# Optimization experiments

Hardware: AMD Instinct MI355X
Metric: run time of the kernel (lower is better)

## Reference

```python
import jax, jax.numpy as jnp
import numpy as np

B, N, K, M, CIN, O, OUT = 4, 1024, 30, 8, 9, 64, 512
BN_SCALE = 1.0 / np.sqrt(1.0 + 1e-5)  # eval-mode BatchNorm with default stats/affine


def setup_inputs() -> dict:
    key = jax.random.key(0)
    ks = jax.random.split(key, 8)
    x = jax.random.normal(ks[0], (B, CIN, N), jnp.float32)
    norm_plt = jax.random.normal(ks[1], (B, 3, N), jnp.float32)
    cls_label = jnp.zeros((B, 16), jnp.float32)
    conv1_w = jax.random.normal(ks[2], (64, 18), jnp.float32) * np.sqrt(2.0 / 18.0)
    conv1_b = jnp.zeros((64,), jnp.float32)
    sn_hw = jax.random.normal(ks[3], (4, 16, 28), jnp.float32) * np.sqrt(2.0 / 28.0)
    sn_ow = jax.random.normal(ks[4], (4, M, 16), jnp.float32) * np.sqrt(2.0 / 16.0)
    sn_ob = jnp.zeros((4, M), jnp.float32)
    mats = jax.random.normal(ks[5], (4, 2 * O, M * O), jnp.float32) * np.sqrt(2.0 / (2.0 * O))
    convt_w = jax.random.normal(ks[6], (OUT, 5 * O), jnp.float32) * np.sqrt(2.0 / (5.0 * O))
    return dict(x=x, norm_plt=norm_plt, cls_label=cls_label, conv1_w=conv1_w,
                conv1_b=conv1_b, sn_hw=sn_hw, sn_ow=sn_ow, sn_ob=sn_ob,
                mats=mats, convt_w=convt_w)


def _gather(feat, idx):
    # feat (B,N,C), idx (B,N,K) int -> (B,N,K,C): neighbor feature gather
    return jax.vmap(lambda f, i: f[i])(feat, idx)


def _bn(t):
    return t * BN_SCALE


def reference(x, norm_plt, cls_label, conv1_w, conv1_b, sn_hw, sn_ow, sn_ob, mats, convt_w):
    xt = jnp.transpose(x, (0, 2, 1))                       # (B,N,9)
    sq = jnp.sum(xt * xt, axis=-1)
    neg_d = 2.0 * jnp.einsum('bic,bjc->bij', xt, xt) - sq[:, :, None] - sq[:, None, :]
    _, idx = jax.lax.top_k(neg_d, K)                       # (B,N,K) knn indices

    nbr = _gather(xt, idx)                                 # (B,N,K,9)
    ctr = jnp.broadcast_to(xt[:, :, None, :], nbr.shape)   # (B,N,K,9)
    diff = nbr - ctr
    ed = jnp.linalg.norm(diff, axis=-1, keepdims=True)     # (B,N,K,1)
    xyz = jnp.concatenate([diff, nbr, ctr, ed], axis=-1)   # (B,N,K,28) scorenet input

    # get_graph_feature -> conv1 (1x1) -> BN -> relu -> max over k
    gf = jnp.concatenate([diff, ctr], axis=-1)             # (B,N,K,18)
    h = jax.nn.relu(_bn(jnp.einsum('bnkc,oc->bnko', gf, conv1_w) + conv1_b))
    x1 = jnp.max(h, axis=2)                                # (B,N,64)

    feats = [x1]
    f = x1
    for l in range(4):  # PAConv layers 2..5 (sequential, fixed count)
        hid = jax.nn.relu(_bn(jnp.einsum('bnkc,hc->bnkh', xyz, sn_hw[l])))
        score = jax.nn.softmax(jnp.einsum('bnkh,mh->bnkm', hid, sn_ow[l]) + sn_ob[l], axis=-1)
        kern = mats[l]                                     # (128, M*64)
        # feat_trans_dgcnn: neighbor uses full kernel on [f;f], center uses top half
        point = (jnp.concatenate([f, f], axis=-1) @ kern).reshape(B, N, M, O)
        center = (f @ kern[:O]).reshape(B, N, M, O)
        # assemble_dgcnn: sum_k sum_m score * (point[knn] - center)
        gp = _gather(point.reshape(B, N, M * O), idx).reshape(B, N, K, M, O)
        out = jnp.einsum('bnkm,bnkmo->bno', score, gp) - jnp.einsum('bnkm,bnmo->bno', score, center)
        f = jax.nn.relu(_bn(out))
        feats.append(f)

    xx = jnp.concatenate(feats, axis=-1)                   # (B,N,320)
    xc = jax.nn.relu(_bn(jnp.einsum('bnc,oc->bno', xx, convt_w)))
    return jnp.max(xc, axis=1)                             # (B,512) global max pool
```

## Files before the change

### kernel.cpp

```cpp
#include <hip/hip_runtime.h>
#include <hip/hip_bf16.h>

#define B 4
#define N 1024
#define KNN 30
#define MM 8
#define OO 64
#define OUTC 512
#define HID 16
#define FD 320
#define BNS 0.9999950000374997f

typedef float f32x4 __attribute__((ext_vector_type(4)));
typedef short s16x8 __attribute__((ext_vector_type(8)));

#define OFF_XT     0
#define OFF_SQ     36864
#define OFF_IDX    40960
#define OFF_CVT    163840
#define OFF_K2T    245760
#define OFF_FB     376832
#define OFF_H      1032192

__global__ void __launch_bounds__(256) k_prep(const float* __restrict__ x,
                                              const float* __restrict__ convt_w,
                                              float* __restrict__ xt,
                                              float* __restrict__ sq,
                                              __hip_bfloat16* __restrict__ cvt_bf,
                                              float* __restrict__ out) {
  int id = blockIdx.x * 256 + threadIdx.x;
  if (id < B * N) {
    int b = id >> 10, n = id & 1023;
    float s = 0.f;
#pragma unroll
    for (int c = 0; c < 9; c++) {
      float v = x[(b * 9 + c) * N + n];
      xt[id * 9 + c] = v;
      s = fmaf(v, v, s);
    }
    sq[id] = s;
  }
  if (id < B * OUTC) out[id] = 0.f;
  if (id < 512 * 320) cvt_bf[id] = __float2bfloat16(convt_w[id]);
}

__global__ void __launch_bounds__(256) k_tpose(const float* __restrict__ mats,
                                               __hip_bfloat16* __restrict__ k2t_bf) {
  int blk = blockIdx.x;
  int l = blk >> 4, part = (blk >> 3) & 1, m = blk & 7;
  __shared__ float tile[64][65];
  int tr = threadIdx.x >> 6;
  int tc = threadIdx.x & 63;
  const float* src = mats + l * 65536 + (part * 64) * 512 + m * 64;
#pragma unroll
  for (int it = 0; it < 16; it++) {
    int c = it * 4 + tr;
    tile[c][tc] = src[c * 512 + tc];
  }
  __syncthreads();
  __hip_bfloat16* dst = k2t_bf + l * 65536 + part * 512 + m * 64;
#pragma unroll
  for (int it = 0; it < 16; it++) {
    int o = it * 4 + tr;
    dst[o * 1024 + tc] = __float2bfloat16(tile[tc][o]);
  }
}

__global__ void __launch_bounds__(256) k_knn(const float* __restrict__ xt,
                                             const float* __restrict__ sq,
                                             int* __restrict__ idx) {
  int r = threadIdx.x >> 6;
  int lane = threadIdx.x & 63;
  int row = blockIdx.x * 4 + r;
  int b = row >> 10;
  __shared__ unsigned int hist[4][256];
  __shared__ unsigned int cntr[4];
  __shared__ unsigned int bp[4];
  __shared__ int bn[4];
  const float* xb = xt + (b << 10) * 9;
  const float* sb = sq + (b << 10);
  float cx[9];
#pragma unroll
  for (int c = 0; c < 9; c++) cx[c] = xt[row * 9 + c];
  float sqn = sq[row];
  unsigned int key[16];
#pragma unroll
  for (int s = 0; s < 16; s++) {
    int j = s * 64 + lane;
    const float* xj = xb + j * 9;
    float dot = 0.f;
#pragma unroll
    for (int c = 0; c < 9; c++) dot = fmaf(cx[c], xj[c], dot);
    float v = 2.0f * dot - sqn - sb[j];
    unsigned int u = __float_as_uint(v);
    key[s] = u ^ ((unsigned int)(((int)u) >> 31) | 0x80000000u);
  }
  if (lane == 0) cntr[r] = 0;
  unsigned int prefix = 0;
  int need = KNN;
  for (int p = 0; p < 4; p++) {
    int shift = 24 - 8 * p;
    for (int i = lane; i < 256; i += 64) hist[r][i] = 0;
    __syncthreads();
    unsigned int himask = (p == 0) ? 0u : (0xFFFFFFFFu << (shift + 8));
#pragma unroll
    for (int s = 0; s < 16; s++) {
      if ((key[s] & himask) == prefix)
        atomicAdd(&hist[r][(key[s] >> shift) & 255], 1u);
    }
    __syncthreads();
    int c0 = hist[r][4 * lane + 0], c1 = hist[r][4 * lane + 1];
    int c2 = hist[r][4 * lane + 2], c3 = hist[r][4 * lane + 3];
    int lsum = c0 + c1 + c2 + c3;
    int sfx = lsum;
#pragma unroll
    for (int ofs = 1; ofs < 64; ofs <<= 1) {
      int t = __shfl_down(sfx, ofs, 64);
      if (lane + ofs < 64) sfx += t;
    }
    int A3 = sfx - lsum;
    int A2 = A3 + c3, A1 = A2 + c2, A0 = A1 + c1;
    if (A0 < need && need <= A0 + c0) { bp[r] = prefix | ((unsigned)(4 * lane + 0) << shift); bn[r] = need - A0; }
    if (A1 < need && need <= A1 + c1) { bp[r] = prefix | ((unsigned)(4 * lane + 1) << shift); bn[r] = need - A1; }
    if (A2 < need && need <= A2 + c2) { bp[r] = prefix | ((unsigned)(4 * lane + 2) << shift); bn[r] = need - A2; }
    if (A3 < need && need <= A3 + c3) { bp[r] = prefix | ((unsigned)(4 * lane + 3) << shift); bn[r] = need - A3; }
    __syncthreads();
    prefix = bp[r];
    need = bn[r];
  }
  unsigned int T = prefix;
  int above_total = KNN - need;
  int* orow = idx + row * KNN;
#pragma unroll
  for (int s = 0; s < 16; s++) {
    if (key[s] > T) {
      unsigned int pslot = atomicAdd(&cntr[r], 1u);
      orow[pslot] = s * 64 + lane;
    }
  }
  int base = 0;
  for (int s = 0; s < 16; s++) {
    unsigned long long m = __ballot(key[s] == T);
    if (key[s] == T) {
      int rk = base + __popcll(m & ((1ull << lane) - 1ull));
      if (rk < need) orow[above_total + rk] = s * 64 + lane;
    }
    base += __popcll(m);
    if (base >= need) break;
  }
}

__global__ void __launch_bounds__(64) k_conv1(const float* __restrict__ xt,
                                              const int* __restrict__ idx,
                                              const float* __restrict__ w,
                                              const float* __restrict__ bias,
                                              __hip_bfloat16* __restrict__ feats_bf) {
  int row = blockIdx.x;
  int t = threadIdx.x;
  int b = row >> 10;
  __shared__ float ws[64 * 18];
  __shared__ __align__(16) float diff_s[KNN][12];
  __shared__ float ctr_s[9];
  for (int i = t; i < 64 * 18; i += 64) ws[i] = w[i];
  if (t < 9) ctr_s[t] = xt[row * 9 + t];
  __syncthreads();
  if (t < KNN) {
    int j = idx[row * KNN + t];
    const float* xj = xt + ((b << 10) + j) * 9;
#pragma unroll
    for (int c = 0; c < 9; c++) diff_s[t][c] = xj[c] - ctr_s[c];
  }
  __syncthreads();
  float wd[9];
#pragma unroll
  for (int c = 0; c < 9; c++) wd[c] = ws[t * 18 + c];
  float cd = 0.f;
#pragma unroll
  for (int c = 0; c < 9; c++) cd = fmaf(ctr_s[c], ws[t * 18 + 9 + c], cd);
  float best = -3.0e38f;
  for (int k = 0; k < KNN; k++) {
    const float4* dr = (const float4*)diff_s[k];
    float4 d0 = dr[0], d1 = dr[1], d2v = dr[2];
    float dd = 0.f;
    dd = fmaf(d0.x, wd[0], dd); dd = fmaf(d0.y, wd[1], dd);
    dd = fmaf(d0.z, wd[2], dd); dd = fmaf(d0.w, wd[3], dd);
    dd = fmaf(d1.x, wd[4], dd); dd = fmaf(d1.y, wd[5], dd);
    dd = fmaf(d1.z, wd[6], dd); dd = fmaf(d1.w, wd[7], dd);
    dd = fmaf(d2v.x, wd[8], dd);
    best = fmaxf(best, dd);
  }
  float val = (best + cd + bias[t]) * BNS;
  feats_bf[row * FD + t] = __float2bfloat16(fmaxf(val, 0.f));
}

__global__ void __launch_bounds__(256) k_g(const float* __restrict__ xt,
                                           const int* __restrict__ idx,
                                           const float* __restrict__ hw,
                                           const float* __restrict__ ow,
                                           const float* __restrict__ ob,
                                           const __hip_bfloat16* __restrict__ feats_bf,
                                           __hip_bfloat16* __restrict__ H, int l) {
  int row0 = blockIdx.x * 4;
  int t = threadIdx.x;
  int b = row0 >> 10;
  __shared__ float hws[HID * 28];
  __shared__ float ows[MM * HID];
  __shared__ float obs[MM];
  __shared__ __align__(16) float sc[4][KNN][8];
  __shared__ __align__(16) float ssum[4][8];
  __shared__ int js[4][KNN];
  __shared__ float ctr[4][9];
  for (int i = t; i < HID * 28; i += 256) hws[i] = hw[l * HID * 28 + i];
  if (t < MM * HID) ows[t] = ow[l * MM * HID + t];
  if (t < MM) obs[t] = ob[l * MM + t];
  if (t < 36) { int r = t / 9, c = t - r * 9; ctr[r][c] = xt[(row0 + r) * 9 + c]; }
  if (t < 4 * KNN) {
    int r = t / KNN, k = t - r * KNN;
    js[r][k] = (b << 10) + idx[(row0 + r) * KNN + k];
  }
  __syncthreads();
  if (t < 4 * KNN) {
    int r = t / KNN, k = t - r * KNN;
    const float* xj = xt + js[r][k] * 9;
    float xv[28];
    float d2 = 0.f;
#pragma unroll
    for (int c = 0; c < 9; c++) {
      float nb = xj[c], ct = ctr[r][c], df = nb - ct;
      xv[c] = df; xv[9 + c] = nb; xv[18 + c] = ct;
      d2 = fmaf(df, df, d2);
    }
    xv[27] = sqrtf(d2);
    float hid[HID];
#pragma unroll
    for (int h = 0; h < HID; h++) {
      float a = 0.f;
#pragma unroll
      for (int c = 0; c < 28; c++) a = fmaf(xv[c], hws[h * 28 + c], a);
      hid[h] = fmaxf(a * BNS, 0.f);
    }
    float lg[MM], mx = -3.0e38f;
#pragma unroll
    for (int m = 0; m < MM; m++) {
      float a = obs[m];
#pragma unroll
      for (int h = 0; h < HID; h++) a = fmaf(hid[h], ows[m * HID + h], a);
      lg[m] = a; mx = fmaxf(mx, a);
    }
    float s = 0.f;
#pragma unroll
    for (int m = 0; m < MM; m++) { lg[m] = __expf(lg[m] - mx); s += lg[m]; }
    float inv = 1.0f / s;
#pragma unroll
    for (int m = 0; m < MM; m++) sc[r][k][m] = lg[m] * inv;
  }
  __syncthreads();
  if (t < 32) {
    int r = t >> 3, m = t & 7;
    float a = 0.f;
#pragma unroll
    for (int k = 0; k < KNN; k++) a += sc[r][k][m];
    ssum[r][m] = a;
  }
  __syncthreads();
  int r = t >> 6, c = t & 63;
  int row = row0 + r;
  float g[MM] = {};
  for (int k = 0; k < KNN; k++) {
    float fv = __bfloat162float(feats_bf[js[r][k] * FD + l * 64 + c]);
    const float4* s4 = (const float4*)sc[r][k];
    float4 s0 = s4[0], s1 = s4[1];
    g[0] = fmaf(s0.x, fv, g[0]); g[1] = fmaf(s0.y, fv, g[1]);
    g[2] = fmaf(s0.z, fv, g[2]); g[3] = fmaf(s0.w, fv, g[3]);
    g[4] = fmaf(s1.x, fv, g[4]); g[5] = fmaf(s1.y, fv, g[5]);
    g[6] = fmaf(s1.z, fv, g[6]); g[7] = fmaf(s1.w, fv, g[7]);
  }
  float fn = __bfloat162float(feats_bf[row * FD + l * 64 + c]);
  __hip_bfloat16* Hrow = H + row * 1024;
#pragma unroll
  for (int m = 0; m < MM; m++) {
    Hrow[m * 64 + c] = __float2bfloat16(g[m] - ssum[r][m] * fn);
    Hrow[512 + m * 64 + c] = __float2bfloat16(g[m]);
  }
}

__global__ void __launch_bounds__(64) k_hgemm(const __hip_bfloat16* __restrict__ H,
                                              const __hip_bfloat16* __restrict__ k2t_bf,
                                              __hip_bfloat16* __restrict__ feats_bf,
                                              int l) {
  int rb = blockIdx.x >> 2, cb = blockIdx.x & 3;
  int row0 = rb * 16, c0 = cb * 16;
  int lane = threadIdx.x;
  int lr = lane & 15, lk8 = (lane >> 4) * 8;
  const short* Hs = (const short*)H;
  const short* Ks = (const short*)(k2t_bf + l * 65536);
  const short* arow = Hs + (row0 + lr) * 1024 + lk8;
  const short* brow = Ks + (c0 + lr) * 1024 + lk8;
  f32x4 acc = {0.f, 0.f, 0.f, 0.f};
#pragma unroll 8
  for (int kk = 0; kk < 32; kk++) {
    s16x8 a = *(const s16x8*)(arow + kk * 32);
    s16x8 bb = *(const s16x8*)(brow + kk * 32);
    acc = __builtin_amdgcn_mfma_f32_16x16x32_bf16(a, bb, acc, 0, 0, 0);
  }
#pragma unroll
  for (int i = 0; i < 4; i++) {
    int row = row0 + (lane >> 4) * 4 + i;
    feats_bf[row * FD + (l + 1) * 64 + c0 + lr] =
        __float2bfloat16(fmaxf(acc[i] * BNS, 0.f));
  }
}

__global__ void __launch_bounds__(256) k_final(const __hip_bfloat16* __restrict__ feats_bf,
                                               const __hip_bfloat16* __restrict__ cvt_bf,
                                               float* __restrict__ out) {
  int m0 = (blockIdx.x >> 1) * 16;
  int nhalf = (blockIdx.x & 1) * 256;
  int w = threadIdx.x >> 6;
  int lane = threadIdx.x & 63;
  int lr = lane & 15, lk8 = (lane >> 4) * 8;
  int b = m0 >> 10;
  const short* Fs = (const short*)feats_bf;
  const short* Ws = (const short*)cvt_bf;
  const short* arow = Fs + (m0 + lr) * FD + lk8;
  int nbase = nhalf + w * 64;
  const short* brow = Ws + (nbase + lr) * FD + lk8;
  f32x4 acc[4] = {{0.f, 0.f, 0.f, 0.f}, {0.f, 0.f, 0.f, 0.f},
                  {0.f, 0.f, 0.f, 0.f}, {0.f, 0.f, 0.f, 0.f}};
#pragma unroll
  for (int kk = 0; kk < 10; kk++) {
    int k0 = kk * 32;
    s16x8 a = *(const s16x8*)(arow + k0);
#pragma unroll
    for (int tn = 0; tn < 4; tn++) {
      s16x8 bb = *(const s16x8*)(brow + tn * 16 * FD + k0);
      acc[tn] = __builtin_amdgcn_mfma_f32_16x16x32_bf16(a, bb, acc[tn], 0, 0, 0);
    }
  }
#pragma unroll
  for (int tn = 0; tn < 4; tn++) {
    float mx = fmaxf(fmaxf(acc[tn][0], acc[tn][1]), fmaxf(acc[tn][2], acc[tn][3]));
    mx = fmaxf(mx, __shfl_xor(mx, 16, 64));
    mx = fmaxf(mx, __shfl_xor(mx, 32, 64));
    if ((lane >> 4) == 0) {
      float val = fmaxf(mx * BNS, 0.f);
      int o = nbase + tn * 16 + lr;
      atomicMax((unsigned int*)out + b * OUTC + o, __float_as_uint(val));
    }
  }
}

extern "C" void kernel_launch(void* const* d_in, const int* in_sizes, int n_in,
                              void* d_out, int out_size, void* d_ws, size_t ws_size,
                              hipStream_t stream) {
  const float* x       = (const float*)d_in[0];
  const float* conv1_w = (const float*)d_in[3];
  const float* conv1_b = (const float*)d_in[4];
  const float* sn_hw   = (const float*)d_in[5];
  const float* sn_ow   = (const float*)d_in[6];
  const float* sn_ob   = (const float*)d_in[7];
  const float* mats    = (const float*)d_in[8];
  const float* convt_w = (const float*)d_in[9];
  float* out = (float*)d_out;

  float* w = (float*)d_ws;
  float* xt = w + OFF_XT;
  float* sq = w + OFF_SQ;
  int* idx = (int*)(w + OFF_IDX);
  __hip_bfloat16* cvt_bf = (__hip_bfloat16*)(w + OFF_CVT);
  __hip_bfloat16* k2t_bf = (__hip_bfloat16*)(w + OFF_K2T);
  __hip_bfloat16* feats_bf = (__hip_bfloat16*)(w + OFF_FB);
  __hip_bfloat16* H = (__hip_bfloat16*)(w + OFF_H);

  k_prep<<<640, 256, 0, stream>>>(x, convt_w, xt, sq, cvt_bf, out);
  k_tpose<<<64, 256, 0, stream>>>(mats, k2t_bf);
  k_knn<<<1024, 256, 0, stream>>>(xt, sq, idx);
  k_conv1<<<4096, 64, 0, stream>>>(xt, idx, conv1_w, conv1_b, feats_bf);
  for (int l = 0; l < 4; l++) {
    k_g<<<1024, 256, 0, stream>>>(xt, idx, sn_hw, sn_ow, sn_ob, feats_bf, H, l);
    k_hgemm<<<1024, 64, 0, stream>>>(H, k2t_bf, feats_bf, l);
  }
  k_final<<<512, 256, 0, stream>>>(feats_bf, cvt_bf, out);
}
```

Measured before the change: 216.0 us.

## Fuse score/gather and H-GEMM into one per-layer kernel with LDS-resident H

Merges k_g and k_hgemm into a single k_layer kernel. Each block handles 16 rows, builds the H tile in shared memory and runs the MFMA GEMM directly from LDS, so the global H round-trip and four launches go away. It also folds the mats transpose into k_prep and batches k_conv1 to 4 rows per 256-thread block to cut launch count and per-block overhead. The cost is fewer blocks per layer (256 instead of 1024) and much larger LDS use, which may lower occupancy and parallelism.

```diff
diff --git a/kernel.cpp b/kernel.cpp
--- a/kernel.cpp
+++ b/kernel.cpp
@@ -20,49 +20,49 @@
 #define OFF_CVT    163840
 #define OFF_K2T    245760
 #define OFF_FB     376832
-#define OFF_H      1032192
 
 __global__ void __launch_bounds__(256) k_prep(const float* __restrict__ x,
                                               const float* __restrict__ convt_w,
+                                              const float* __restrict__ mats,
                                               float* __restrict__ xt,
                                               float* __restrict__ sq,
                                               __hip_bfloat16* __restrict__ cvt_bf,
+                                              __hip_bfloat16* __restrict__ k2t_bf,
                                               float* __restrict__ out) {
-  int id = blockIdx.x * 256 + threadIdx.x;
-  if (id < B * N) {
-    int b = id >> 10, n = id & 1023;
-    float s = 0.f;
-#pragma unroll
-    for (int c = 0; c < 9; c++) {
-      float v = x[(b * 9 + c) * N + n];
-      xt[id * 9 + c] = v;
-      s = fmaf(v, v, s);
-    }
-    sq[id] = s;
-  }
-  if (id < B * OUTC) out[id] = 0.f;
-  if (id < 512 * 320) cvt_bf[id] = __float2bfloat16(convt_w[id]);
-}
-
-__global__ void __launch_bounds__(256) k_tpose(const float* __restrict__ mats,
-                                               __hip_bfloat16* __restrict__ k2t_bf) {
-  int blk = blockIdx.x;
-  int l = blk >> 4, part = (blk >> 3) & 1, m = blk & 7;
   __shared__ float tile[64][65];
-  int tr = threadIdx.x >> 6;
-  int tc = threadIdx.x & 63;
-  const float* src = mats + l * 65536 + (part * 64) * 512 + m * 64;
-#pragma unroll
-  for (int it = 0; it < 16; it++) {
-    int c = it * 4 + tr;
-    tile[c][tc] = src[c * 512 + tc];
-  }
-  __syncthreads();
-  __hip_bfloat16* dst = k2t_bf + l * 65536 + part * 512 + m * 64;
-#pragma unroll
-  for (int it = 0; it < 16; it++) {
-    int o = it * 4 + tr;
-    dst[o * 1024 + tc] = __float2bfloat16(tile[tc][o]);
+  if (blockIdx.x < 640) {
+    int id = blockIdx.x * 256 + threadIdx.x;
+    if (id < B * N) {
+      int b = id >> 10, n = id & 1023;
+      float s = 0.f;
+#pragma unroll
+      for (int c = 0; c < 9; c++) {
+        float v = x[(b * 9 + c) * N + n];
+        xt[id * 9 + c] = v;
+        s = fmaf(v, v, s);
+      }
+      sq[id] = s;
+    }
+    if (id < B * OUTC) out[id] = 0.f;
+    if (id < 512 * 320) cvt_bf[id] = __float2bfloat16(convt_w[id]);
+  } else {
+    int blk = blockIdx.x - 640;
+    int l = blk >> 4, part = (blk >> 3) & 1, m = blk & 7;
+    int tr = threadIdx.x >> 6;
+    int tc = threadIdx.x & 63;
+    const float* src = mats + l * 65536 + (part * 64) * 512 + m * 64;
+#pragma unroll
+    for (int it = 0; it < 16; it++) {
+      int c = it * 4 + tr;
+      tile[c][tc] = src[c * 512 + tc];
+    }
+    __syncthreads();
+    __hip_bfloat16* dst = k2t_bf + l * 65536 + part * 512 + m * 64;
+#pragma unroll
+    for (int it = 0; it < 16; it++) {
+      int o = it * 4 + tr;
+      dst[o * 1024 + tc] = __float2bfloat16(tile[tc][o]);
+    }
   }
 }
 
@@ -150,36 +150,39 @@
   }
 }
 
-__global__ void __launch_bounds__(64) k_conv1(const float* __restrict__ xt,
-                                              const int* __restrict__ idx,
-                                              const float* __restrict__ w,
-                                              const float* __restrict__ bias,
-                                              __hip_bfloat16* __restrict__ feats_bf) {
-  int row = blockIdx.x;
+__global__ void __launch_bounds__(256) k_conv1(const float* __restrict__ xt,
+                                               const int* __restrict__ idx,
+                                               const float* __restrict__ w,
+                                               const float* __restrict__ bias,
+                                               __hip_bfloat16* __restrict__ feats_bf) {
+  int row0 = blockIdx.x * 4;
   int t = threadIdx.x;
-  int b = row >> 10;
+  int b = row0 >> 10;
   __shared__ float ws[64 * 18];
-  __shared__ __align__(16) float diff_s[KNN][12];
-  __shared__ float ctr_s[9];
-  for (int i = t; i < 64 * 18; i += 64) ws[i] = w[i];
-  if (t < 9) ctr_s[t] = xt[row * 9 + t];
-  __syncthreads();
-  if (t < KNN) {
-    int j = idx[row * KNN + t];
+  __shared__ __align__(16) float diff_s[4][KNN][12];
+  __shared__ float ctr_s[4][9];
+  for (int i = t; i < 64 * 18; i += 256) ws[i] = w[i];
+  if (t < 36) { int r = t / 9, c = t - r * 9; ctr_s[r][c] = xt[(row0 + r) * 9 + c]; }
+  __syncthreads();
+  if (t < 120) {
+    int r = t / KNN, k = t - r * KNN;
+    int j = idx[(row0 + r) * KNN + k];
     const float* xj = xt + ((b << 10) + j) * 9;
 #pragma unroll
-    for (int c = 0; c < 9; c++) diff_s[t][c] = xj[c] - ctr_s[c];
-  }
-  __syncthreads();
+    for (int c = 0; c < 9; c++) diff_s[r][k][c] = xj[c] - ctr_s[r][c];
+  }
+  __syncthreads();
+  int wv = t >> 6, lane = t & 63;
+  int row = row0 + wv;
   float wd[9];
 #pragma unroll
-  for (int c = 0; c < 9; c++) wd[c] = ws[t * 18 + c];
+  for (int c = 0; c < 9; c++) wd[c] = ws[lane * 18 + c];
   float cd = 0.f;
 #pragma unroll
-  for (int c = 0; c < 9; c++) cd = fmaf(ctr_s[c], ws[t * 18 + 9 + c], cd);
+  for (int c = 0; c < 9; c++) cd = fmaf(ctr_s[wv][c], ws[lane * 18 + 9 + c], cd);
   float best = -3.0e38f;
   for (int k = 0; k < KNN; k++) {
-    const float4* dr = (const float4*)diff_s[k];
+    const float4* dr = (const float4*)diff_s[wv][k];
     float4 d0 = dr[0], d1 = dr[1], d2v = dr[2];
     float dd = 0.f;
     dd = fmaf(d0.x, wd[0], dd); dd = fmaf(d0.y, wd[1], dd);
@@ -189,38 +192,40 @@
     dd = fmaf(d2v.x, wd[8], dd);
     best = fmaxf(best, dd);
   }
-  float val = (best + cd + bias[t]) * BNS;
-  feats_bf[row * FD + t] = __float2bfloat16(fmaxf(val, 0.f));
-}
-
-__global__ void __launch_bounds__(256) k_g(const float* __restrict__ xt,
-                                           const int* __restrict__ idx,
-                                           const float* __restrict__ hw,
-                                           const float* __restrict__ ow,
-                                           const float* __restrict__ ob,
-                                           const __hip_bfloat16* __restrict__ feats_bf,
-                                           __hip_bfloat16* __restrict__ H, int l) {
-  int row0 = blockIdx.x * 4;
+  float val = (best + cd + bias[lane]) * BNS;
+  feats_bf[row * FD + lane] = __float2bfloat16(fmaxf(val, 0.f));
+}
+
+__global__ void __launch_bounds__(256) k_layer(const float* __restrict__ xt,
+                                               const int* __restrict__ idx,
+                                               const float* __restrict__ hw,
+                                               const float* __restrict__ ow,
+                                               const float* __restrict__ ob,
+                                               const __hip_bfloat16* __restrict__ k2t_bf,
+                                               __hip_bfloat16* __restrict__ feats_bf,
+                                               int l) {
+  int row0 = blockIdx.x * 16;
   int t = threadIdx.x;
   int b = row0 >> 10;
   __shared__ float hws[HID * 28];
   __shared__ float ows[MM * HID];
   __shared__ float obs[MM];
-  __shared__ __align__(16) float sc[4][KNN][8];
-  __shared__ __align__(16) float ssum[4][8];
-  __shared__ int js[4][KNN];
-  __shared__ float ctr[4][9];
+  __shared__ int js[16][KNN];
+  __shared__ float ctr[16][9];
+  __shared__ __align__(16) float sc[16][KNN][8];
+  __shared__ float ssum[16][8];
+  __shared__ __align__(16) __hip_bfloat16 Hs[16][1040];
   for (int i = t; i < HID * 28; i += 256) hws[i] = hw[l * HID * 28 + i];
   if (t < MM * HID) ows[t] = ow[l * MM * HID + t];
   if (t < MM) obs[t] = ob[l * MM + t];
-  if (t < 36) { int r = t / 9, c = t - r * 9; ctr[r][c] = xt[(row0 + r) * 9 + c]; }
-  if (t < 4 * KNN) {
-    int r = t / KNN, k = t - r * KNN;
+  if (t < 144) { int r = t / 9, c = t - r * 9; ctr[r][c] = xt[(row0 + r) * 9 + c]; }
+  for (int i = t; i < 16 * KNN; i += 256) {
+    int r = i / KNN, k = i - r * KNN;
     js[r][k] = (b << 10) + idx[(row0 + r) * KNN + k];
   }
   __syncthreads();
-  if (t < 4 * KNN) {
-    int r = t / KNN, k = t - r * KNN;
+  for (int i = t; i < 16 * KNN; i += 256) {
+    int r = i / KNN, k = i - r * KNN;
     const float* xj = xt + js[r][k] * 9;
     float xv[28];
     float d2 = 0.f;
@@ -255,7 +260,7 @@
     for (int m = 0; m < MM; m++) sc[r][k][m] = lg[m] * inv;
   }
   __syncthreads();
-  if (t < 32) {
+  if (t < 128) {
     int r = t >> 3, m = t & 7;
     float a = 0.f;
 #pragma unroll
@@ -263,39 +268,34 @@
     ssum[r][m] = a;
   }
   __syncthreads();
-  int r = t >> 6, c = t & 63;
-  int row = row0 + r;
-  float g[MM] = {};
-  for (int k = 0; k < KNN; k++) {
-    float fv = __bfloat162float(feats_bf[js[r][k] * FD + l * 64 + c]);
-    const float4* s4 = (const float4*)sc[r][k];
-    float4 s0 = s4[0], s1 = s4[1];
-    g[0] = fmaf(s0.x, fv, g[0]); g[1] = fmaf(s0.y, fv, g[1]);
-    g[2] = fmaf(s0.z, fv, g[2]); g[3] = fmaf(s0.w, fv, g[3]);
-    g[4] = fmaf(s1.x, fv, g[4]); g[5] = fmaf(s1.y, fv, g[5]);
-    g[6] = fmaf(s1.z, fv, g[6]); g[7] = fmaf(s1.w, fv, g[7]);
-  }
-  float fn = __bfloat162float(feats_bf[row * FD + l * 64 + c]);
-  __hip_bfloat16* Hrow = H + row * 1024;
-#pragma unroll
-  for (int m = 0; m < MM; m++) {
-    Hrow[m * 64 + c] = __float2bfloat16(g[m] - ssum[r][m] * fn);
-    Hrow[512 + m * 64 + c] = __float2bfloat16(g[m]);
-  }
-}
-
-__global__ void __launch_bounds__(64) k_hgemm(const __hip_bfloat16* __restrict__ H,
-                                              const __hip_bfloat16* __restrict__ k2t_bf,
-                                              __hip_bfloat16* __restrict__ feats_bf,
-                                              int l) {
-  int rb = blockIdx.x >> 2, cb = blockIdx.x & 3;
-  int row0 = rb * 16, c0 = cb * 16;
-  int lane = threadIdx.x;
+  int wv = t >> 6, lane = t & 63;
+#pragma unroll
+  for (int rr = 0; rr < 4; rr++) {
+    int r = wv * 4 + rr;
+    int row = row0 + r;
+    float g[MM] = {};
+#pragma unroll
+    for (int k = 0; k < KNN; k++) {
+      float fv = __bfloat162float(feats_bf[js[r][k] * FD + l * 64 + lane]);
+      const float4* s4 = (const float4*)sc[r][k];
+      float4 s0 = s4[0], s1 = s4[1];
+      g[0] = fmaf(s0.x, fv, g[0]); g[1] = fmaf(s0.y, fv, g[1]);
+      g[2] = fmaf(s0.z, fv, g[2]); g[3] = fmaf(s0.w, fv, g[3]);
+      g[4] = fmaf(s1.x, fv, g[4]); g[5] = fmaf(s1.y, fv, g[5]);
+      g[6] = fmaf(s1.z, fv, g[6]); g[7] = fmaf(s1.w, fv, g[7]);
+    }
+    float fn = __bfloat162float(feats_bf[row * FD + l * 64 + lane]);
+#pragma unroll
+    for (int m = 0; m < MM; m++) {
+      Hs[r][m * 64 + lane] = __float2bfloat16(g[m] - ssum[r][m] * fn);
+      Hs[r][512 + m * 64 + lane] = __float2bfloat16(g[m]);
+    }
+  }
+  __syncthreads();
   int lr = lane & 15, lk8 = (lane >> 4) * 8;
-  const short* Hs = (const short*)H;
-  const short* Ks = (const short*)(k2t_bf + l * 65536);
-  const short* arow = Hs + (row0 + lr) * 1024 + lk8;
-  const short* brow = Ks + (c0 + lr) * 1024 + lk8;
+  const short* Ks2 = (const short*)(k2t_bf + l * 65536);
+  const short* brow = Ks2 + (wv * 16 + lr) * 1024 + lk8;
+  const short* arow = (const short*)&Hs[lr][lk8];
   f32x4 acc = {0.f, 0.f, 0.f, 0.f};
 #pragma unroll 8
   for (int kk = 0; kk < 32; kk++) {
@@ -306,7 +306,7 @@
 #pragma unroll
   for (int i = 0; i < 4; i++) {
     int row = row0 + (lane >> 4) * 4 + i;
-    feats_bf[row * FD + (l + 1) * 64 + c0 + lr] =
+    feats_bf[row * FD + (l + 1) * 64 + wv * 16 + lr] =
         __float2bfloat16(fmaxf(acc[i] * BNS, 0.f));
   }
 }
@@ -370,15 +370,12 @@
   __hip_bfloat16* cvt_bf = (__hip_bfloat16*)(w + OFF_CVT);
   __hip_bfloat16* k2t_bf = (__hip_bfloat16*)(w + OFF_K2T);
   __hip_bfloat16* feats_bf = (__hip_bfloat16*)(w + OFF_FB);
-  __hip_bfloat16* H = (__hip_bfloat16*)(w + OFF_H);
-
-  k_prep<<<640, 256, 0, stream>>>(x, convt_w, xt, sq, cvt_bf, out);
-  k_tpose<<<64, 256, 0, stream>>>(mats, k2t_bf);
+
+  k_prep<<<704, 256, 0, stream>>>(x, convt_w, mats, xt, sq, cvt_bf, k2t_bf, out);
   k_knn<<<1024, 256, 0, stream>>>(xt, sq, idx);
-  k_conv1<<<4096, 64, 0, stream>>>(xt, idx, conv1_w, conv1_b, feats_bf);
+  k_conv1<<<1024, 256, 0, stream>>>(xt, idx, conv1_w, conv1_b, feats_bf);
   for (int l = 0; l < 4; l++) {
-    k_g<<<1024, 256, 0, stream>>>(xt, idx, sn_hw, sn_ow, sn_ob, feats_bf, H, l);
-    k_hgemm<<<1024, 64, 0, stream>>>(H, k2t_bf, feats_bf, l);
+    k_layer<<<256, 256, 0, stream>>>(xt, idx, sn_hw, sn_ow, sn_ob, k2t_bf, feats_bf, l);
   }
   k_final<<<512, 256, 0, stream>>>(feats_bf, cvt_bf, out);
 }
```

New measurement: 208.0 us. -3.7%, faster.
